# Kernel optimization log

Measured on AMD Instinct MI355X. Metric: run time of the kernel, lower is better.

Reference implementation:

```python
import jax, jax.numpy as jnp
import numpy as np

N_HEAD = 8
D_HEAD = 128   # dim_k = dim_q = dim_v
SEG_LEN = 512
EPS = 1e-6


def setup_inputs() -> dict:
    key = jax.random.key(0)
    ks = jax.random.split(key, 8)
    B, T, D = 2, 4096, 1024
    scale = 0.02
    x = jax.random.normal(ks[0], (B, T, D), dtype=jnp.float32)
    w_q = jax.random.normal(ks[1], (D, N_HEAD * D_HEAD), dtype=jnp.float32) * scale
    w_k = jax.random.normal(ks[2], (D, N_HEAD * D_HEAD), dtype=jnp.float32) * scale
    w_v = jax.random.normal(ks[3], (D, N_HEAD * D_HEAD), dtype=jnp.float32) * scale
    b_q = jnp.zeros((N_HEAD * D_HEAD,), jnp.float32)
    b_k = jnp.zeros((N_HEAD * D_HEAD,), jnp.float32)
    b_v = jnp.zeros((N_HEAD * D_HEAD,), jnp.float32)
    beta = jnp.zeros((N_HEAD,), jnp.float32)
    return {"x": x, "w_q": w_q, "b_q": b_q, "w_k": w_k, "b_k": b_k,
            "w_v": w_v, "b_v": b_v, "beta": beta}


def _heads(y, B, T):
    # [B,T,H*D] -> [B,H,T,D]
    return y.reshape(B, T, N_HEAD, D_HEAD).transpose(0, 2, 1, 3)


def reference(x, w_q, b_q, w_k, b_k, w_v, b_v, beta):
    B, T, _ = x.shape
    S = T // SEG_LEN
    q = _heads(x @ w_q + b_q, B, T)
    k = _heads(x @ w_k + b_k, B, T)
    v = _heads(x @ w_v + b_v, B, T)

    # segment: [B,H,T,D] -> [S,B,H,L,D]
    def seg(y):
        return y.reshape(B, N_HEAD, S, SEG_LEN, D_HEAD).transpose(2, 0, 1, 3, 4)
    qs, ks_, vs = seg(q), seg(k), seg(v)

    causal = jnp.tril(jnp.ones((SEG_LEN, SEG_LEN), bool))
    gate = jax.nn.sigmoid(beta).reshape(1, N_HEAD, 1, 1)
    inv_sqrt_d = 1.0 / jnp.sqrt(jnp.asarray(D_HEAD, x.dtype))

    def step(carry, segdat):
        M, z = carry                      # M: [B,H,Dk,Dv], z: [B,H,Dk]
        qc, kc, vc = segdat               # [B,H,L,D]
        sq = jax.nn.elu(qc) + 1.0
        sk = jax.nn.elu(kc) + 1.0
        # retrieval from memory BEFORE update
        a_mem = jnp.einsum('bhld,bhde->bhle', sq, M) / (
            jnp.einsum('bhld,bhd->bhl', sq, z)[..., None] + EPS)
        # delta-rule memory update
        retr_k = jnp.einsum('bhld,bhde->bhle', sk, M) / (
            jnp.einsum('bhld,bhd->bhl', sk, z)[..., None] + EPS)
        M = M + jnp.einsum('bhld,bhle->bhde', sk, vc - retr_k)
        z = z + sk.sum(axis=2)
        # local causal dot-product attention within the segment
        scores = jnp.einsum('bhld,bhmd->bhlm', qc, kc) * inv_sqrt_d
        scores = jnp.where(causal, scores, jnp.asarray(-1e30, scores.dtype))
        a_dot = jnp.einsum('bhlm,bhmd->bhld', jax.nn.softmax(scores, axis=-1), vc)
        # long-term context injection
        a = gate * a_mem + (1.0 - gate) * a_dot
        return (M, z), a

    M0 = jnp.zeros((B, N_HEAD, D_HEAD, D_HEAD), x.dtype)
    z0 = jnp.zeros((B, N_HEAD, D_HEAD), x.dtype)
    _, out = jax.lax.scan(step, (M0, z0), (qs, ks_, vs))
    # [S,B,H,L,D] -> [B,T,H*D]
    out = out.transpose(1, 3, 0, 2, 4).reshape(B, T, N_HEAD * D_HEAD)
    # wait: axes of out are [S,B,H,L,D]; reorder to [B,S,L,H,D]
    return out


# fix ordering: define reference properly (overrides above draft path)
def reference(x, w_q, b_q, w_k, b_k, w_v, b_v, beta):
    B, T, _ = x.shape
    S = T // SEG_LEN
    q = _heads(x @ w_q + b_q, B, T)
    k = _heads(x @ w_k + b_k, B, T)
    v = _heads(x @ w_v + b_v, B, T)

    def seg(y):
        return y.reshape(B, N_HEAD, S, SEG_LEN, D_HEAD).transpose(2, 0, 1, 3, 4)
    qs, ks_, vs = seg(q), seg(k), seg(v)

    causal = jnp.tril(jnp.ones((SEG_LEN, SEG_LEN), bool))
    gate = jax.nn.sigmoid(beta).reshape(1, N_HEAD, 1, 1)
    inv_sqrt_d = 1.0 / jnp.sqrt(jnp.asarray(D_HEAD, x.dtype))

    def step(carry, segdat):
        M, z = carry
        qc, kc, vc = segdat
        sq = jax.nn.elu(qc) + 1.0
        sk = jax.nn.elu(kc) + 1.0
        a_mem = jnp.einsum('bhld,bhde->bhle', sq, M) / (
            jnp.einsum('bhld,bhd->bhl', sq, z)[..., None] + EPS)
        retr_k = jnp.einsum('bhld,bhde->bhle', sk, M) / (
            jnp.einsum('bhld,bhd->bhl', sk, z)[..., None] + EPS)
        M = M + jnp.einsum('bhld,bhle->bhde', sk, vc - retr_k)
        z = z + sk.sum(axis=2)
        scores = jnp.einsum('bhld,bhmd->bhlm', qc, kc) * inv_sqrt_d
        scores = jnp.where(causal, scores, jnp.asarray(-1e30, scores.dtype))
        a_dot = jnp.einsum('bhlm,bhmd->bhld', jax.nn.softmax(scores, axis=-1), vc)
        a = gate * a_mem + (1.0 - gate) * a_dot
        return (M, z), a

    M0 = jnp.zeros((B, N_HEAD, D_HEAD, D_HEAD), x.dtype)
    z0 = jnp.zeros((B, N_HEAD, D_HEAD), x.dtype)
    _, out = jax.lax.scan(step, (M0, z0), (qs, ks_, vs))  # [S,B,H,L,D]
    out = out.transpose(1, 0, 3, 2, 4).reshape(B, T, N_HEAD * D_HEAD)
    return out
```

## Files before the change

kernel.cpp:

```cpp
#include <hip/hip_runtime.h>
#include <hip/hip_bf16.h>

typedef __attribute__((ext_vector_type(8))) short bf16x8;
typedef __attribute__((ext_vector_type(4))) float f32x4;
typedef unsigned short u16;
typedef unsigned int u32;

#define DEV static __device__ __forceinline__

DEV float bf2f(u16 u){ u32 x = ((u32)u)<<16; float f; __builtin_memcpy(&f,&x,4); return f; }
DEV u16 f2bf(float f){ u32 x; __builtin_memcpy(&x,&f,4); return (u16)((x + 0x7fffu + ((x>>16)&1u))>>16); }
DEV float elu1(float x){ return x > 0.f ? x + 1.f : __expf(x); }

DEV void gload16(const u16* g, u16* l){
  __builtin_amdgcn_global_load_lds(
      (const __attribute__((address_space(1))) unsigned int*)(g),
      (__attribute__((address_space(3))) unsigned int*)(l), 16, 0, 0);
}

#define MFMA(a,b,c) __builtin_amdgcn_mfma_f32_16x16x32_bf16((a),(b),(c),0,0,0)

#define NB 2
#define NT 4096
#define NH 8
#define DH 128
#define NS 8
#define SL 512
#define ND 1024
#define N3 3072
#define EPS 1e-6f

__global__ __launch_bounds__(256) void k_xc(const float* __restrict__ x, u16* __restrict__ xb){
  int i = blockIdx.x*256 + threadIdx.x;
  const float4 v0 = *(const float4*)(x + (size_t)i*8);
  const float4 v1 = *(const float4*)(x + (size_t)i*8 + 4);
  bf16x8 o;
  o[0]=(short)f2bf(v0.x); o[1]=(short)f2bf(v0.y); o[2]=(short)f2bf(v0.z); o[3]=(short)f2bf(v0.w);
  o[4]=(short)f2bf(v1.x); o[5]=(short)f2bf(v1.y); o[6]=(short)f2bf(v1.z); o[7]=(short)f2bf(v1.w);
  *(bf16x8*)(xb + (size_t)i*8) = o;
}

__global__ __launch_bounds__(256) void k_wt(const float* __restrict__ wq,
                                            const float* __restrict__ wk,
                                            const float* __restrict__ wv,
                                            u16* __restrict__ wt,
                                            float* __restrict__ cs){
  __shared__ float t[32][33];
  const int z = blockIdx.z;
  const float* w = (z==0) ? wq : (z==1 ? wk : wv);
  const int k0 = blockIdx.x*32, n0 = blockIdx.y*32;
  const int tx = threadIdx.x, ty = threadIdx.y;
  if (z==0 && blockIdx.x==0 && blockIdx.y==0){
    const int tid = ty*32 + tx;
#pragma unroll
    for (int i=0;i<64;i++) cs[tid + i*256] = 0.f;
  }
#pragma unroll
  for (int i=0;i<4;i++) t[ty+i*8][tx] = w[(size_t)(k0+ty+i*8)*ND + n0+tx];
  __syncthreads();
#pragma unroll
  for (int i=0;i<4;i++)
    wt[(size_t)(z*ND + n0+ty+i*8)*ND + k0+tx] = f2bf(t[tx][ty+i*8]);
}

__global__ __launch_bounds__(256) void k_gemm(const u16* __restrict__ xb,
                                              const u16* __restrict__ wt,
                                              const float* __restrict__ bq,
                                              const float* __restrict__ bk,
                                              const float* __restrict__ bv,
                                              u16* __restrict__ qkv){
  __shared__ __align__(16) u16 As[128*64];
  __shared__ __align__(16) u16 Bs[128*64];
  const int m0 = blockIdx.x*128, n0 = blockIdx.y*128;
  const int tid = threadIdx.x;
  const int w = tid>>6, lane = tid&63, g = lane>>4, li = lane&15;
  const int wr = w>>1, wc = w&1;
  const int srow = lane>>3;
  const int ssl  = (lane&7) ^ srow;
  f32x4 z4 = {0.f,0.f,0.f,0.f};
  f32x4 acc[4][4];
#pragma unroll
  for (int mi=0;mi<4;mi++)
#pragma unroll
    for (int ni=0;ni<4;ni++) acc[mi][ni] = z4;

  for (int kt=0; kt<16; ++kt){
    const int k0 = kt*64;
#pragma unroll
    for (int i=0;i<4;i++){
      const int c = i*4 + w;
      const int row = c*8 + srow;
      gload16(xb + (size_t)(m0+row)*ND + k0 + ssl*8, As + c*512);
      gload16(wt + (size_t)(n0+row)*ND + k0 + ssl*8, Bs + c*512);
    }
    __syncthreads();
#pragma unroll
    for (int kk=0;kk<2;kk++){
      bf16x8 a[4], bb[4];
#pragma unroll
      for (int mi=0;mi<4;mi++){
        int row = wr*64 + mi*16 + li;
        int slot = kk*4 + g;
        a[mi] = *(const bf16x8*)(As + row*64 + ((slot^(row&7))<<3));
      }
#pragma unroll
      for (int ni=0;ni<4;ni++){
        int row = wc*64 + ni*16 + li;
        int slot = kk*4 + g;
        bb[ni] = *(const bf16x8*)(Bs + row*64 + ((slot^(row&7))<<3));
      }
#pragma unroll
      for (int mi=0;mi<4;mi++)
#pragma unroll
        for (int ni=0;ni<4;ni++)
          acc[mi][ni] = MFMA(a[mi], bb[ni], acc[mi][ni]);
    }
    __syncthreads();
  }

  u16* SC = (w < 2 ? As : Bs) + (w&1)*4096;
#pragma unroll
  for (int ni=0;ni<4;ni++){
    const int n = n0 + wc*64 + ni*16 + li;
    const float bias = (n < ND) ? bq[n] : (n < 2*ND ? bk[n-ND] : bv[n-2*ND]);
#pragma unroll
    for (int mi=0;mi<4;mi++)
#pragma unroll
      for (int rr=0;rr<4;rr++){
        const int ml = mi*16 + 4*g + rr;
        const int nl = ni*16 + li;
        SC[ml*64 + (((nl>>3)^(ml&7))<<3) + (nl&7)] = f2bf(acc[mi][ni][rr] + bias);
      }
  }
  __syncthreads();
  const int rb = lane>>3, cb = lane&7;
#pragma unroll
  for (int j=0;j<8;j++){
    const int r = j*8 + rb;
    bf16x8 v = *(const bf16x8*)(SC + r*64 + ((cb^(r&7))<<3));
    *(bf16x8*)(qkv + (size_t)(m0 + wr*64 + r)*N3 + n0 + wc*64 + cb*8) = v;
  }
}

__global__ __launch_bounds__(256) void k_tr(const u16* __restrict__ qkv,
                                            u16* __restrict__ vt,
                                            u16* __restrict__ pkT,
                                            float* __restrict__ cs){
  __shared__ __align__(4) u16 t[64*66];
  __shared__ float pf[8][64];
  const int t0 = blockIdx.x*64, d0 = blockIdx.y*64;
  const int z = blockIdx.z, bh = z>>1, part = z&1;
  const int b = bh>>3, h = bh&7;
  const int basec = (part ? 2*ND : ND) + h*DH;
  const int tid = threadIdx.x;
  float s0 = 0.f, s1 = 0.f;
#pragma unroll
  for (int i=0;i<8;i++){
    int fp = tid + i*256;
    int row = fp>>5, c2 = (fp&31)*2;
    ushort2 v = *(const ushort2*)(qkv + (size_t)(b*NT + t0+row)*N3 + basec + d0 + c2);
    if (!part){
      float e0 = elu1(bf2f(v.x)), e1 = elu1(bf2f(v.y));
      s0 += e0; s1 += e1;
      v.x = f2bf(e0); v.y = f2bf(e1);
    }
    *(ushort2*)(t + row*66 + c2) = v;
  }
  if (!part){ pf[tid>>5][(tid&31)*2] = s0; pf[tid>>5][(tid&31)*2+1] = s1; }
  __syncthreads();
  u16* dst = part ? vt : pkT;
#pragma unroll
  for (int i=0;i<8;i++){
    int fp = tid + i*256;
    int dr = fp>>5, c2 = (fp&31)*2;
    ushort2 v; v.x = t[c2*66 + dr]; v.y = t[(c2+1)*66 + dr];
    *(ushort2*)(dst + (size_t)(bh*DH + d0+dr)*NT + t0 + c2) = v;
  }
  if (!part && tid < 64){
    float a = 0.f;
#pragma unroll
    for (int r=0;r<8;r++) a += pf[r][tid];
    const int bhs = b*64 + h*8 + (t0>>9);
    atomicAdd(&cs[(size_t)bhs*DH + d0 + tid], a);
  }
}

__global__ __launch_bounds__(512) void k_dinv(const u16* __restrict__ qkv,
                                              const float* __restrict__ cs,
                                              float* __restrict__ dinvK){
  const int bhs = blockIdx.x, half = blockIdx.y;
  const int b = bhs>>6, h = (bhs>>3)&7, s = bhs&7;
  const int tid = threadIdx.x, w = tid>>6, lane = tid&63, grp = lane>>4, li = lane&15;
  __shared__ float zl[128];
  if (tid < 128){
    float a = 0.f;
    for (int sp=0; sp<s; ++sp) a += cs[(size_t)(bhs - s + sp)*DH + tid];
    zl[tid] = a;
  }
  __syncthreads();
#pragma unroll
  for (int it=0; it<8; ++it){
    const int r = half*256 + w*32 + it*4 + grp;
    bf16x8 v = *(const bf16x8*)(qkv + (size_t)(b*NT + s*SL + r)*N3 + ND + h*DH + li*8);
    float p = 0.f;
#pragma unroll
    for (int j=0;j<8;j++) p += elu1(bf2f((u16)v[j])) * zl[li*8+j];
    p += __shfl_xor(p,1); p += __shfl_xor(p,2);
    p += __shfl_xor(p,4); p += __shfl_xor(p,8);
    if (li == 0) dinvK[(size_t)bhs*SL + r] = 1.f/(p + EPS);
  }
}

__global__ __launch_bounds__(512) void k_gram(const u16* __restrict__ pkT,
                                              const u16* __restrict__ vtb,
                                              const float* __restrict__ dinvK,
                                              u16* __restrict__ G, float* __restrict__ Bm){
  const int bhs = blockIdx.x, ec = blockIdx.y;
  const int bh = bhs>>3, s = bhs&7, tb = s*SL;
  const int tid = threadIdx.x, w = tid>>6, lane = tid&63, g = lane>>4, li = lane&15;
  __shared__ __align__(16) u16 Bk[32*512];
  __shared__ __align__(16) u16 Bv[32*512];
  __shared__ float dv[512];
  dv[tid] = dinvK[(size_t)bhs*SL + tid];
#pragma unroll
  for (int i=0;i<4;i++){
    const int ee = i*8 + w;
    const size_t rowo = ((size_t)bh*DH + ec*32 + ee)*NT + tb + ((lane^w)<<3);
    gload16(pkT + rowo, Bk + ee*512);
    gload16(vtb + rowo, Bv + ee*512);
  }
  __syncthreads();
  f32x4 z4 = {0.f,0.f,0.f,0.f};
  f32x4 Ga[2] = {z4,z4}, Ba[2] = {z4,z4};
  const u16* arow = pkT + ((size_t)bh*DH + 16*w + li)*NT + tb;
  for (int ks=0; ks<16; ++ks){
    const int r0 = ks*32 + g*8;
    bf16x8 araw = *(const bf16x8*)(arow + r0);
    float4 d0 = *(const float4*)(dv + r0);
    float4 d1 = *(const float4*)(dv + r0 + 4);
    bf16x8 ascl;
    ascl[0] = (short)f2bf(bf2f((u16)araw[0]) * d0.x);
    ascl[1] = (short)f2bf(bf2f((u16)araw[1]) * d0.y);
    ascl[2] = (short)f2bf(bf2f((u16)araw[2]) * d0.z);
    ascl[3] = (short)f2bf(bf2f((u16)araw[3]) * d0.w);
    ascl[4] = (short)f2bf(bf2f((u16)araw[4]) * d1.x);
    ascl[5] = (short)f2bf(bf2f((u16)araw[5]) * d1.y);
    ascl[6] = (short)f2bf(bf2f((u16)araw[6]) * d1.z);
    ascl[7] = (short)f2bf(bf2f((u16)araw[7]) * d1.w);
    const int slot = ks*4 + g;
#pragma unroll
    for (int ni=0;ni<2;ni++){
      const int ee = ni*16 + li;
      bf16x8 bk8 = *(const bf16x8*)(Bk + ee*512 + ((slot^(li&7))<<3));
      bf16x8 bv8 = *(const bf16x8*)(Bv + ee*512 + ((slot^(li&7))<<3));
      Ga[ni] = MFMA(ascl, bk8, Ga[ni]);
      Ba[ni] = MFMA(araw, bv8, Ba[ni]);
    }
  }
#pragma unroll
  for (int ni=0;ni<2;ni++)
#pragma unroll
    for (int rr=0;rr<4;rr++){
      const int dd = 16*w + 4*g + rr;
      const int ee = ec*32 + ni*16 + li;
      G[((size_t)bhs*DH + dd)*DH + ee] = f2bf(Ga[ni][rr]);
      Bm[((size_t)bhs*DH + dd)*DH + ee] = Ba[ni][rr];
    }
}

__global__ __launch_bounds__(512) void k_scan(const u16* __restrict__ G,
                                              const float* __restrict__ Bm,
                                              u16* __restrict__ MTs){
  const int bh = blockIdx.x, ec = blockIdx.y;
  const int tid = threadIdx.x, w = tid>>6, lane = tid&63, g = lane>>4, li = lane&15;
  __shared__ float MF[16*132];
  __shared__ __align__(16) u16 MB[16*128];
  for (int i = tid; i < 16*132; i += 512) MF[i] = 0.f;
  __syncthreads();
  const int dr = w*16 + li;
  for (int s=0;s<NS;s++){
    const size_t bhs = (size_t)bh*NS + s;
    if (tid < 256){
      const int e = tid>>4, dg = tid&15;
      const float* src = MF + e*132 + dg*8;
      bf16x8 v;
#pragma unroll
      for (int j=0;j<8;j++) v[j] = (short)f2bf(src[j]);
      *(bf16x8*)(MTs + bhs*16384 + (size_t)(ec*16+e)*128 + dg*8) = v;
      *(bf16x8*)(MB + e*128 + ((dg^(e&7))<<3)) = v;
    }
    __syncthreads();
    f32x4 acc = {0.f,0.f,0.f,0.f};
#pragma unroll
    for (int ks=0;ks<4;ks++){
      bf16x8 a = *(const bf16x8*)(G + ((size_t)bhs*DH + dr)*DH + ks*32 + g*8);
      const int sl = ks*4 + g;
      bf16x8 bfr = *(const bf16x8*)(MB + li*128 + ((sl^(li&7))<<3));
      acc = MFMA(a, bfr, acc);
    }
#pragma unroll
    for (int rr=0;rr<4;rr++){
      const int d = w*16 + 4*g + rr;
      const float delta = Bm[((size_t)bhs*DH + d)*DH + ec*16 + li] - acc[rr];
      MF[li*132 + d] += delta;
    }
    __syncthreads();
  }
}

__global__ __launch_bounds__(512) void k_attn(const u16* __restrict__ qkv,
                                              const u16* __restrict__ vtb,
                                              const u16* __restrict__ MTs,
                                              const float* __restrict__ cs,
                                              const float* __restrict__ beta,
                                              float* __restrict__ out){
  const int bhs = blockIdx.x, half = blockIdx.y;
  const int b = bhs>>6, h = (bhs>>3)&7, s = bhs&7, bh = bhs>>3;
  const int tid = threadIdx.x, w = tid>>6, lane = tid&63, g = lane>>4, li = lane&15;
  const int jq = (w < 4) ? (half + 2*w) : (15 - half - 2*(w-4));
  const int qb = jq*32;
  const float gate = 1.f/(1.f + __expf(-beta[h]));
  const float isd = 0.08838834764831845f;
  const float L2E = 1.4426950408889634f;
  __shared__ __align__(16) u16 P[8*1024];
  __shared__ float zl[128];
  __shared__ float dinvW[8][32];
  u16* Pw = P + w*1024;

  if (tid < 128){
    float a = 0.f;
    for (int sp=0; sp<s; ++sp) a += cs[(size_t)(bhs - s + sp)*DH + tid];
    zl[tid] = a;
  }
  __syncthreads();

  {
    const int r = qb + (lane&31);
    const int dh = (lane>>5)*64;
    const u16* qrow = qkv + (size_t)(b*NT + s*SL + r)*N3 + h*DH + dh;
    float p = 0.f;
#pragma unroll
    for (int j=0;j<64;j+=8){
      bf16x8 v = *(const bf16x8*)(qrow + j);
#pragma unroll
      for (int t=0;t<8;t++) p += elu1(bf2f((u16)v[t])) * zl[dh + j + t];
    }
    p += __shfl_xor(p, 32);
    if (lane < 32) dinvW[w][lane] = 1.f/(p + EPS);
  }

  bf16x8 qf[2][4];
#pragma unroll
  for (int mf=0; mf<2; ++mf)
#pragma unroll
    for (int kf=0; kf<4; ++kf)
      qf[mf][kf] = *(const bf16x8*)(qkv + (size_t)(b*NT + s*SL + qb + mf*16 + li)*N3 + h*DH + kf*32 + g*8);

  f32x4 z4 = {0.f,0.f,0.f,0.f};
  f32x4 O[2][8];
  float lr[2][4];
#pragma unroll
  for (int mf=0;mf<2;++mf){
#pragma unroll
    for (int nf=0;nf<8;++nf) O[mf][nf] = z4;
#pragma unroll
    for (int rr=0;rr<4;++rr) lr[mf][rr] = 0.f;
  }

  const int nch = jq + 1;
  for (int c=0; c<nch; ++c){
    const int kb = c*32;
    f32x4 sa[2][2];
#pragma unroll
    for (int mf=0;mf<2;++mf)
#pragma unroll
      for (int nf=0;nf<2;++nf) sa[mf][nf] = z4;
#pragma unroll
    for (int kf=0; kf<4; ++kf)
#pragma unroll
      for (int nf=0; nf<2; ++nf){
        bf16x8 bk8 = *(const bf16x8*)(qkv + (size_t)(b*NT + s*SL + kb + nf*16 + li)*N3 + ND + h*DH + kf*32 + g*8);
        sa[0][nf] = MFMA(qf[0][kf], bk8, sa[0][nf]);
        sa[1][nf] = MFMA(qf[1][kf], bk8, sa[1][nf]);
      }
    float pv[2][2][4];
#pragma unroll
    for (int mf=0;mf<2;++mf)
#pragma unroll
      for (int rr=0;rr<4;++rr){
        int row = qb + mf*16 + 4*g + rr;
        float rs = 0.f;
#pragma unroll
        for (int nf=0;nf<2;++nf){
          int col = kb + nf*16 + li;
          float sc = sa[mf][nf][rr]*isd;
          float p = (col > row) ? 0.f : exp2f(sc*L2E);
          pv[mf][nf][rr] = p; rs += p;
        }
        rs += __shfl_xor(rs, 1); rs += __shfl_xor(rs, 2);
        rs += __shfl_xor(rs, 4); rs += __shfl_xor(rs, 8);
        lr[mf][rr] += rs;
      }
#pragma unroll
    for (int mf=0;mf<2;++mf)
#pragma unroll
      for (int nf=0;nf<2;++nf)
#pragma unroll
        for (int rr=0;rr<4;++rr){
          int row = mf*16 + 4*g + rr, col = nf*16 + li;
          Pw[row*32 + (((col>>3)^(row&3))<<3) + (col&7)] = f2bf(pv[mf][nf][rr]);
        }
    bf16x8 pa[2];
#pragma unroll
    for (int mf=0;mf<2;++mf){
      int row = mf*16 + li;
      pa[mf] = *(const bf16x8*)(Pw + row*32 + ((g^(row&3))<<3));
    }
#pragma unroll
    for (int nf=0;nf<8;++nf){
      bf16x8 bv8 = *(const bf16x8*)(vtb + ((size_t)bh*DH + nf*16 + li)*NT + s*SL + kb + g*8);
      O[0][nf] = MFMA(pa[0], bv8, O[0][nf]);
      O[1][nf] = MFMA(pa[1], bv8, O[1][nf]);
    }
  }

  f32x4 Am[2][8];
#pragma unroll
  for (int mf=0;mf<2;++mf)
#pragma unroll
    for (int nf=0;nf<8;++nf) Am[mf][nf] = z4;
#pragma unroll
  for (int ks=0;ks<4;++ks){
    bf16x8 pq[2];
#pragma unroll
    for (int mf=0;mf<2;++mf){
      bf16x8 raw = qf[mf][ks];
#pragma unroll
      for (int j=0;j<8;j++) raw[j] = (short)f2bf(elu1(bf2f((u16)raw[j])));
      pq[mf] = raw;
    }
#pragma unroll
    for (int nf=0;nf<8;++nf){
      bf16x8 bfr = *(const bf16x8*)(MTs + ((size_t)bhs*DH + nf*16 + li)*DH + ks*32 + g*8);
      Am[0][nf] = MFMA(pq[0], bfr, Am[0][nf]);
      Am[1][nf] = MFMA(pq[1], bfr, Am[1][nf]);
    }
  }

  const float og = 1.f - gate;
#pragma unroll
  for (int mf=0;mf<2;++mf)
#pragma unroll
    for (int rr=0;rr<4;++rr){
      int row = qb + mf*16 + 4*g + rr;
      float invd = og / lr[mf][rr];
      float dv = gate * dinvW[w][row - qb];
#pragma unroll
      for (int nf=0;nf<8;++nf)
        out[(size_t)(b*NT + s*SL + row)*ND + h*DH + nf*16 + li] =
            O[mf][nf][rr]*invd + Am[mf][nf][rr]*dv;
    }
}

extern "C" void kernel_launch(void* const* d_in, const int* in_sizes, int n_in,
                              void* d_out, int out_size, void* d_ws, size_t ws_size,
                              hipStream_t stream) {
  (void)in_sizes; (void)n_in; (void)out_size; (void)ws_size;
  const float* x    = (const float*)d_in[0];
  const float* wq   = (const float*)d_in[1];
  const float* bq   = (const float*)d_in[2];
  const float* wk   = (const float*)d_in[3];
  const float* bk   = (const float*)d_in[4];
  const float* wv   = (const float*)d_in[5];
  const float* bv   = (const float*)d_in[6];
  const float* beta = (const float*)d_in[7];
  float* out = (float*)d_out;
  char* ws = (char*)d_ws;

  u16*   wt  = (u16*)  (ws + 0);
  u16*   qkv = (u16*)  (ws + 6291456);
  u16*   vt  = (u16*)  (ws + 56623104);
  u16*   pkT = (u16*)  (ws + 73400320);
  u16*   G   = (u16*)  (ws + 90177536);
  float* Bm  = (float*)(ws + 94371840);
  u16*   MTs = (u16*)  (ws + 102760448);
  float* cs  = (float*)(ws + 106954752);
  u16*   xb  = vt;
  float* dinvK = (float*)(ws + 107020288);

  hipLaunchKernelGGL(k_xc,    dim3(4096),    dim3(256),  0, stream, x, xb);
  hipLaunchKernelGGL(k_wt,    dim3(32,32,3), dim3(32,8), 0, stream, wq, wk, wv, wt, cs);
  hipLaunchKernelGGL(k_gemm,  dim3(64,24),   dim3(256),  0, stream, xb, wt, bq, bk, bv, qkv);
  hipLaunchKernelGGL(k_tr,    dim3(64,2,32), dim3(256),  0, stream, qkv, vt, pkT, cs);
  hipLaunchKernelGGL(k_dinv,  dim3(128,2),   dim3(512),  0, stream, qkv, cs, dinvK);
  hipLaunchKernelGGL(k_gram,  dim3(128,4),   dim3(512),  0, stream, pkT, vt, dinvK, G, Bm);
  hipLaunchKernelGGL(k_scan,  dim3(16,8),    dim3(512),  0, stream, G, Bm, MTs);
  hipLaunchKernelGGL(k_attn,  dim3(128,2),   dim3(512),  0, stream, qkv, vt, MTs, cs, beta, out);
}
```

Baseline: 186.5 us.

## Fuse transpose and ELU column-sum into QKV GEMM epilogue, drop k_tr kernel

The separate transpose kernel is removed. The GEMM epilogue now writes transposed ELU+1 keys and transposed values directly through swizzled LDS, and accumulates per-segment column sums with shuffles and atomics. This saves one kernel launch and a full re-read of the K and V parts of qkv from global memory. In exchange the GEMM epilogue grows, and xb is moved to a separate workspace region so it no longer aliases vt.

Measured after the change: 175.7 us. 5.8% less time.

```diff
diff --git a/kernel.cpp b/kernel.cpp
--- a/kernel.cpp
+++ b/kernel.cpp
@@ -68,7 +68,10 @@
                                               const float* __restrict__ bq,
                                               const float* __restrict__ bk,
                                               const float* __restrict__ bv,
-                                              u16* __restrict__ qkv){
+                                              u16* __restrict__ qkv,
+                                              u16* __restrict__ pkTo,
+                                              u16* __restrict__ vto,
+                                              float* __restrict__ cs){
   __shared__ __align__(16) u16 As[128*64];
   __shared__ __align__(16) u16 Bs[128*64];
   const int m0 = blockIdx.x*128, n0 = blockIdx.y*128;
@@ -118,70 +121,80 @@
     __syncthreads();
   }
 
-  u16* SC = (w < 2 ? As : Bs) + (w&1)*4096;
-#pragma unroll
-  for (int ni=0;ni<4;ni++){
-    const int n = n0 + wc*64 + ni*16 + li;
-    const float bias = (n < ND) ? bq[n] : (n < 2*ND ? bk[n-ND] : bv[n-2*ND]);
-#pragma unroll
-    for (int mi=0;mi<4;mi++)
-#pragma unroll
-      for (int rr=0;rr<4;rr++){
-        const int ml = mi*16 + 4*g + rr;
-        const int nl = ni*16 + li;
-        SC[ml*64 + (((nl>>3)^(ml&7))<<3) + (nl&7)] = f2bf(acc[mi][ni][rr] + bias);
+  const int part = n0 >> 10;
+  const int hh = (n0 >> 7) & 7;
+  const int bb2 = m0 >> 12;
+  const int tloc = m0 & (NT-1);
+  const int rb = lane>>3, cb = lane&7;
+  u16* SCw = (w < 2 ? As : Bs) + (w&1)*4096;
+
+  if (part < 2){
+#pragma unroll
+    for (int ni=0;ni<4;ni++){
+      const int n = n0 + wc*64 + ni*16 + li;
+      const float bias = (part==0) ? bq[n] : bk[n-ND];
+#pragma unroll
+      for (int mi=0;mi<4;mi++)
+#pragma unroll
+        for (int rr=0;rr<4;rr++){
+          const int ml = mi*16 + 4*g + rr;
+          const int nl = ni*16 + li;
+          SCw[ml*64 + (((nl>>3)^(ml&7))<<3) + (nl&7)] = f2bf(acc[mi][ni][rr] + bias);
+        }
+    }
+    __syncthreads();
+#pragma unroll
+    for (int j=0;j<8;j++){
+      const int r = j*8 + rb;
+      bf16x8 v = *(const bf16x8*)(SCw + r*64 + ((cb^(r&7))<<3));
+      *(bf16x8*)(qkv + (size_t)(m0 + wr*64 + r)*N3 + n0 + wc*64 + cb*8) = v;
+    }
+  }
+  if (part >= 1){
+    __syncthreads();
+    float csum[4] = {0.f,0.f,0.f,0.f};
+#pragma unroll
+    for (int ni=0;ni<4;ni++){
+      const int n = n0 + wc*64 + ni*16 + li;
+      const float bias = (part==1) ? bk[n-ND] : bv[n-2*ND];
+      const int nl = ni*16 + li;
+#pragma unroll
+      for (int mi=0;mi<4;mi++){
+        float v0 = acc[mi][ni][0] + bias;
+        float v1 = acc[mi][ni][1] + bias;
+        float v2 = acc[mi][ni][2] + bias;
+        float v3 = acc[mi][ni][3] + bias;
+        if (part==1){
+          v0 = elu1(v0); v1 = elu1(v1); v2 = elu1(v2); v3 = elu1(v3);
+          csum[ni] += v0+v1+v2+v3;
+        }
+        short4 pk;
+        pk.x = (short)f2bf(v0); pk.y = (short)f2bf(v1);
+        pk.z = (short)f2bf(v2); pk.w = (short)f2bf(v3);
+        const int gran = (2*mi + (g>>1)) ^ (nl&7);
+        *(short4*)(SCw + nl*64 + (gran<<3) + 4*(g&1)) = pk;
       }
-  }
-  __syncthreads();
-  const int rb = lane>>3, cb = lane&7;
-#pragma unroll
-  for (int j=0;j<8;j++){
-    const int r = j*8 + rb;
-    bf16x8 v = *(const bf16x8*)(SC + r*64 + ((cb^(r&7))<<3));
-    *(bf16x8*)(qkv + (size_t)(m0 + wr*64 + r)*N3 + n0 + wc*64 + cb*8) = v;
-  }
-}
-
-__global__ __launch_bounds__(256) void k_tr(const u16* __restrict__ qkv,
-                                            u16* __restrict__ vt,
-                                            u16* __restrict__ pkT,
-                                            float* __restrict__ cs){
-  __shared__ __align__(4) u16 t[64*66];
-  __shared__ float pf[8][64];
-  const int t0 = blockIdx.x*64, d0 = blockIdx.y*64;
-  const int z = blockIdx.z, bh = z>>1, part = z&1;
-  const int b = bh>>3, h = bh&7;
-  const int basec = (part ? 2*ND : ND) + h*DH;
-  const int tid = threadIdx.x;
-  float s0 = 0.f, s1 = 0.f;
-#pragma unroll
-  for (int i=0;i<8;i++){
-    int fp = tid + i*256;
-    int row = fp>>5, c2 = (fp&31)*2;
-    ushort2 v = *(const ushort2*)(qkv + (size_t)(b*NT + t0+row)*N3 + basec + d0 + c2);
-    if (!part){
-      float e0 = elu1(bf2f(v.x)), e1 = elu1(bf2f(v.y));
-      s0 += e0; s1 += e1;
-      v.x = f2bf(e0); v.y = f2bf(e1);
-    }
-    *(ushort2*)(t + row*66 + c2) = v;
-  }
-  if (!part){ pf[tid>>5][(tid&31)*2] = s0; pf[tid>>5][(tid&31)*2+1] = s1; }
-  __syncthreads();
-  u16* dst = part ? vt : pkT;
-#pragma unroll
-  for (int i=0;i<8;i++){
-    int fp = tid + i*256;
-    int dr = fp>>5, c2 = (fp&31)*2;
-    ushort2 v; v.x = t[c2*66 + dr]; v.y = t[(c2+1)*66 + dr];
-    *(ushort2*)(dst + (size_t)(bh*DH + d0+dr)*NT + t0 + c2) = v;
-  }
-  if (!part && tid < 64){
-    float a = 0.f;
-#pragma unroll
-    for (int r=0;r<8;r++) a += pf[r][tid];
-    const int bhs = b*64 + h*8 + (t0>>9);
-    atomicAdd(&cs[(size_t)bhs*DH + d0 + tid], a);
+    }
+    __syncthreads();
+    u16* dstT = (part==1) ? pkTo : vto;
+    const int bh = bb2*8 + hh;
+#pragma unroll
+    for (int j=0;j<8;j++){
+      const int r = j*8 + rb;
+      bf16x8 v = *(const bf16x8*)(SCw + r*64 + ((cb^(r&7))<<3));
+      *(bf16x8*)(dstT + (size_t)(bh*DH + wc*64 + r)*NT + tloc + wr*64 + cb*8) = v;
+    }
+    if (part==1){
+      const int s = tloc >> 9;
+      const int bhs = bb2*64 + hh*8 + s;
+#pragma unroll
+      for (int ni=0;ni<4;ni++){
+        float c = csum[ni];
+        c += __shfl_xor(c,16); c += __shfl_xor(c,32);
+        if (g==0)
+          atomicAdd(&cs[(size_t)bhs*DH + wc*64 + ni*16 + li], c);
+      }
+    }
   }
 }
 
@@ -485,13 +498,12 @@
   float* Bm  = (float*)(ws + 94371840);
   u16*   MTs = (u16*)  (ws + 102760448);
   float* cs  = (float*)(ws + 106954752);
-  u16*   xb  = vt;
   float* dinvK = (float*)(ws + 107020288);
+  u16*   xb  = (u16*)  (ws + 90177536);
 
   hipLaunchKernelGGL(k_xc,    dim3(4096),    dim3(256),  0, stream, x, xb);
   hipLaunchKernelGGL(k_wt,    dim3(32,32,3), dim3(32,8), 0, stream, wq, wk, wv, wt, cs);
-  hipLaunchKernelGGL(k_gemm,  dim3(64,24),   dim3(256),  0, stream, xb, wt, bq, bk, bv, qkv);
-  hipLaunchKernelGGL(k_tr,    dim3(64,2,32), dim3(256),  0, stream, qkv, vt, pkT, cs);
+  hipLaunchKernelGGL(k_gemm,  dim3(64,24),   dim3(256),  0, stream, xb, wt, bq, bk, bv, qkv, pkT, vt, cs);
   hipLaunchKernelGGL(k_dinv,  dim3(128,2),   dim3(512),  0, stream, qkv, cs, dinvK);
   hipLaunchKernelGGL(k_gram,  dim3(128,4),   dim3(512),  0, stream, pkT, vt, dinvK, G, Bm);
   hipLaunchKernelGGL(k_scan,  dim3(16,8),    dim3(512),  0, stream, G, Bm, MTs);
```
